# Kernel optimization log

Measured on AMD Instinct MI355X. Metric: run time of the kernel, lower is better.

The kernel has to match this reference:

```python
import jax, jax.numpy as jnp
import numpy as np

B, N, DI, DS, DP, DM, S = 64, 4096, 64, 64, 64, 128, 7
NUM_ITER = 3
EPS_ATTN = 1e-8
LN_EPS = 1e-5


def setup_inputs() -> dict:
    key = jax.random.key(0)
    ks = jax.random.split(key, 12)
    rn = lambda k, shp, sc=1.0: (jax.random.normal(k, shp, jnp.float32) * sc)
    return {
        "x": rn(ks[0], (B, N, DI)),
        "ln_inp_g": jnp.ones((DI,), jnp.float32),
        "ln_inp_b": jnp.zeros((DI,), jnp.float32),
        "ln_slot_g": jnp.ones((DS,), jnp.float32),
        "ln_slot_b": jnp.zeros((DS,), jnp.float32),
        "slots_init": rn(ks[1], (1, S, DS)),
        "Wk": rn(ks[2], (DI, DP), 1.0 / np.sqrt(DI)),
        "Wv": rn(ks[3], (DI, DP), 1.0 / np.sqrt(DI)),
        "Wq": rn(ks[4], (DS, DP), 1.0 / np.sqrt(DS)),
        "gru_wih": rn(ks[5], (3 * DS, DP), 1.0 / np.sqrt(DS)),
        "gru_whh": rn(ks[6], (3 * DS, DS), 1.0 / np.sqrt(DS)),
        "gru_bih": jnp.zeros((3 * DS,), jnp.float32),
        "gru_bhh": jnp.zeros((3 * DS,), jnp.float32),
        "mlp_w1": rn(ks[7], (DS, DM), 1.0 / np.sqrt(DS)),
        "mlp_b1": jnp.zeros((DM,), jnp.float32),
        "mlp_w2": rn(ks[8], (DM, DS), 1.0 / np.sqrt(DM)),
        "mlp_b2": jnp.zeros((DS,), jnp.float32),
    }


def _layernorm(x, g, b):
    m = jnp.mean(x, axis=-1, keepdims=True)
    v = jnp.mean(jnp.square(x - m), axis=-1, keepdims=True)
    return (x - m) * jax.lax.rsqrt(v + LN_EPS) * g + b


def _gru_cell(u, h, wih, whh, bih, bhh):
    # PyTorch GRUCell semantics
    gi = u @ wih.T + bih  # [*, 3*DS]
    gh = h @ whh.T + bhh
    ir, iz, inn = jnp.split(gi, 3, axis=-1)
    hr, hz, hn = jnp.split(gh, 3, axis=-1)
    r = jax.nn.sigmoid(ir + hr)
    z = jax.nn.sigmoid(iz + hz)
    n = jnp.tanh(inn + r * hn)
    return (1.0 - z) * n + z * h


def reference(x, ln_inp_g, ln_inp_b, ln_slot_g, ln_slot_b, slots_init,
              Wk, Wv, Wq, gru_wih, gru_whh, gru_bih, gru_bhh,
              mlp_w1, mlp_b1, mlp_w2, mlp_b2):
    x = _layernorm(x, ln_inp_g, ln_inp_b)          # [B,N,DI]
    k = x @ Wk                                      # [B,N,DP] (hoisted; x fixed across iters)
    v = x @ Wv                                      # [B,N,DP]
    slots = jnp.broadcast_to(slots_init, (x.shape[0], S, DS))
    scale = 1.0 / np.sqrt(DP)
    for _ in range(NUM_ITER):
        slots_prev = slots
        sn = _layernorm(slots, ln_slot_g, ln_slot_b)
        q = sn @ Wq                                 # [B,S,DP]
        attn = jnp.einsum('bnd,bsd->bns', k, q) * scale
        attn = jax.nn.softmax(attn, axis=-1) + EPS_ATTN      # softmax over slots
        weights = attn / jnp.sum(attn, axis=1, keepdims=True)  # normalize over N
        updates = jnp.einsum('bns,bnd->bsd', weights, v)     # [B,S,DP]
        h = _gru_cell(updates.reshape(-1, DP), slots_prev.reshape(-1, DS),
                      gru_wih, gru_whh, gru_bih, gru_bhh)
        slots = h.reshape(-1, S, DS)
        slots = slots + (jax.nn.relu(slots @ mlp_w1 + mlp_b1) @ mlp_w2 + mlp_b2)
    return slots
```

## Files before the change

### kernel.cpp

```cpp
#include <hip/hip_runtime.h>
#include <stdint.h>

#define L2E 1.44269504088896f

static __device__ __forceinline__ float wsum(float v) {
    #pragma unroll
    for (int m = 1; m < 64; m <<= 1) v += __shfl_xor(v, m, 64);
    return v;
}
static __device__ __forceinline__ float sigm(float x) {
    return 1.0f / (1.0f + __builtin_amdgcn_exp2f(-x * L2E));
}
static __device__ __forceinline__ float tanh_(float x) {
    const float ax = fabsf(x);
    const float t = __builtin_amdgcn_exp2f(-2.0f * ax * L2E);
    const float r = (1.0f - t) / (1.0f + t);
    return (x < 0.f) ? -r : r;
}

__global__ __launch_bounds__(256) void transpose_kernel(
    const float* __restrict__ wih, const float* __restrict__ whh,
    const float* __restrict__ Wk,
    float* __restrict__ wihT, float* __restrict__ whhT, float* __restrict__ WkT)
{
    const int idx = blockIdx.x * 256 + threadIdx.x;
    if (idx < 12288) {
        const int i = idx / 192, j = idx - i * 192;
        wihT[idx] = wih[j * 64 + i];
    } else if (idx < 24576) {
        const int o = idx - 12288;
        const int i = o / 192, j = o - i * 192;
        whhT[o] = whh[j * 64 + i];
    } else {
        const int o = idx - 24576;
        const int p = o >> 6, d = o & 63;
        WkT[o] = Wk[d * 64 + p];
    }
}

static __device__ __forceinline__ void slot_ln_q_kq(
    float snv, int wv, int lane, int r,
    float* scr, const float* wkT,
    const float* lsg, const float* lsb, const float* Wq,
    const float* lig, const float* lib,
    float* __restrict__ gkq, float* __restrict__ aux)
{
    const float mean = wsum(snv) * (1.0f / 64.0f);
    const float d = snv - mean;
    const float var = wsum(d * d) * (1.0f / 64.0f);
    const float rs = rsqrtf(var + 1e-5f);
    const float sn = d * rs * lsg[lane] + lsb[lane];
    __syncthreads();
    scr[lane] = sn;
    __syncthreads();
    float q = 0.f;
    #pragma unroll 8
    for (int i = 0; i < 64; ++i) q = fmaf(scr[i], Wq[i * 64 + lane], q);
    q *= 0.125f;
    __syncthreads();
    scr[lane] = q;
    __syncthreads();
    float kq = 0.f;
    #pragma unroll 8
    for (int p = 0; p < 64; ++p) kq = fmaf(wkT[p * 64 + lane], scr[p], kq);
    const float bk = wsum(lib[lane] * kq);
    const float gk = lig[lane] * kq;
    const float g1 = wsum(gk);
    gkq[r * 64 + lane] = gk;
    if (lane == 0) { aux[r * 2] = g1; aux[r * 2 + 1] = bk; }
}

__global__ __launch_bounds__(256) void init_kernel(
    const float* __restrict__ s0,
    const float* __restrict__ lsg, const float* __restrict__ lsb,
    const float* __restrict__ Wq,  const float* __restrict__ Wk,
    const float* __restrict__ lig, const float* __restrict__ lib,
    float* __restrict__ slots, float* __restrict__ gkq, float* __restrict__ aux)
{
    __shared__ float wkT[4096];
    __shared__ float scr[4][64];
    const int tid = threadIdx.x, lane = tid & 63, wv = tid >> 6;
    const int r = blockIdx.x * 4 + wv;
    const int s = r % 7;
    #pragma unroll
    for (int i = tid; i < 4096; i += 256) {
        const int d = i >> 6, p = i & 63;
        wkT[p * 64 + d] = Wk[i];
    }
    const float h = s0[s * 64 + lane];
    slots[r * 64 + lane] = h;
    __syncthreads();
    slot_ln_q_kq(h, wv, lane, r, &scr[wv][0], wkT, lsg, lsb, Wq, lig, lib, gkq, aux);
}

__global__ __launch_bounds__(256) void attn_kernel(
    const float* __restrict__ x,
    const float* __restrict__ gkq, const float* __restrict__ aux,
    float* __restrict__ Ypart)
{
    __shared__ float xsh[4][32 * 65];
    __shared__ float wsh[4][32][8];
    __shared__ float gkql[448];
    __shared__ float auxl[14];
    __shared__ float ybuf[4][456];
    const int tid = threadIdx.x, lane = tid & 63, wv = tid >> 6;
    const int b = blockIdx.x >> 4, chunk = blockIdx.x & 15;

    gkql[tid] = gkq[b * 448 + tid];
    if (tid < 192) gkql[tid + 256] = gkq[b * 448 + tid + 256];
    if (tid < 14) auxl[tid] = aux[b * 14 + tid];
    __syncthreads();

    const int q5 = lane & 31, h = lane >> 5;
    float Yr[14];
    #pragma unroll
    for (int i = 0; i < 14; ++i) Yr[i] = 0.f;
    float cacc[7] = {0.f, 0.f, 0.f, 0.f, 0.f, 0.f, 0.f};

    const float* tbase = x + (((long)b * 4096) + chunk * 256 + wv * 64) * 64;
    #pragma unroll 1
    for (int pass = 0; pass < 2; ++pass) {
        const float4* src = (const float4*)(tbase + pass * 2048);
        #pragma unroll
        for (int st = 0; st < 8; ++st) {
            const float4 d4 = src[st * 64 + lane];
            const int f = (st * 64 + lane) * 4;
            const int row = f >> 6, dim = f & 63;
            float* dst = &xsh[wv][row * 65 + dim];
            dst[0] = d4.x; dst[1] = d4.y; dst[2] = d4.z; dst[3] = d4.w;
        }

        float xf[32];
        float sum = 0.f, ss = 0.f;
        const float* xr = &xsh[wv][q5 * 65 + h * 32];
        #pragma unroll
        for (int c = 0; c < 32; ++c) {
            xf[c] = xr[c];
            sum += xf[c];
            ss = fmaf(xf[c], xf[c], ss);
        }
        float acc[7];
        #pragma unroll
        for (int s = 0; s < 7; ++s) {
            float a = 0.f;
            const float* gk = &gkql[s * 64 + h * 32];
            #pragma unroll
            for (int c = 0; c < 32; ++c) a = fmaf(xf[c], gk[c], a);
            acc[s] = a;
        }
        sum += __shfl_xor(sum, 32, 64);
        ss  += __shfl_xor(ss, 32, 64);
        #pragma unroll
        for (int s = 0; s < 7; ++s) acc[s] += __shfl_xor(acc[s], 32, 64);

        const float m   = sum * (1.0f / 64.0f);
        const float var = ss * (1.0f / 64.0f) - m * m;
        const float rs  = rsqrtf(var + 1e-5f);
        const float rsm = rs * m;
        float t[7];
        #pragma unroll
        for (int s = 0; s < 7; ++s)
            t[s] = fmaf(rs, acc[s], fmaf(-rsm, auxl[2 * s], auxl[2 * s + 1]));
        float mx = t[0];
        #pragma unroll
        for (int s = 1; s < 7; ++s) mx = fmaxf(mx, t[s]);
        float e[7], se = 0.f;
        #pragma unroll
        for (int s = 0; s < 7; ++s) {
            e[s] = __builtin_amdgcn_exp2f((t[s] - mx) * L2E);
            se += e[s];
        }
        const float inv = 1.0f / se;
        #pragma unroll
        for (int s = 0; s < 7; ++s) {
            const float w = fmaf(e[s], inv, 1e-8f);
            cacc[s] += w;
            if (h == 0) wsh[wv][q5][s] = w * rs;
        }
        if (h == 0) wsh[wv][q5][7] = 0.f;

        #pragma unroll 4
        for (int r2 = 0; r2 < 16; ++r2) {
            const int rr = r2 * 2 + h;
            const float4 p0 = *(const float4*)&wsh[wv][rr][0];
            const float4 p1 = *(const float4*)&wsh[wv][rr][4];
            const float v0 = xsh[wv][rr * 65 + q5 * 2];
            const float v1 = xsh[wv][rr * 65 + q5 * 2 + 1];
            const float ps[7] = {p0.x, p0.y, p0.z, p0.w, p1.x, p1.y, p1.z};
            #pragma unroll
            for (int s = 0; s < 7; ++s) {
                Yr[2 * s]     = fmaf(ps[s], v0, Yr[2 * s]);
                Yr[2 * s + 1] = fmaf(ps[s], v1, Yr[2 * s + 1]);
            }
        }
    }

    #pragma unroll
    for (int i = 0; i < 14; ++i) Yr[i] += __shfl_xor(Yr[i], 32, 64);
    if (h == 0) {
        #pragma unroll
        for (int s = 0; s < 7; ++s) {
            ybuf[wv][s * 64 + q5 * 2]     = Yr[2 * s];
            ybuf[wv][s * 64 + q5 * 2 + 1] = Yr[2 * s + 1];
        }
    }
    #pragma unroll
    for (int s = 0; s < 7; ++s) {
        const float Cs = wsum(cacc[s]) * 0.5f;
        if (lane == 0) ybuf[wv][448 + s] = Cs;
    }
    if (lane == 1) ybuf[wv][455] = 0.f;
    __syncthreads();
    for (int i = tid; i < 456; i += 256)
        Ypart[((long)b * 16 + chunk) * 456 + i] =
            ybuf[0][i] + ybuf[1][i] + ybuf[2][i] + ybuf[3][i];
}

__global__ __launch_bounds__(256) void update_kernel(
    const float* __restrict__ Ypart, float* __restrict__ slots,
    const float* __restrict__ Wv,
    const float* __restrict__ wihT, const float* __restrict__ whhT,
    const float* __restrict__ bih,  const float* __restrict__ bhh,
    const float* __restrict__ w1,   const float* __restrict__ b1,
    const float* __restrict__ w2,   const float* __restrict__ b2,
    const float* __restrict__ lsg,  const float* __restrict__ lsb,
    const float* __restrict__ Wq,   const float* __restrict__ WkT,
    const float* __restrict__ lig,  const float* __restrict__ lib,
    float* __restrict__ gkq, float* __restrict__ aux,
    float* __restrict__ out, int last)
{
    __shared__ float red[4][64];
    __shared__ float c16[16];
    __shared__ float ash[64];
    __shared__ float ush[64];
    __shared__ float hsh[64];
    __shared__ float gish[192], ghsh[192];
    __shared__ float hnsh[64];
    __shared__ float mbsh[128];
    __shared__ float qsh[64];
    const int tid = threadIdx.x, lane = tid & 63, wv = tid >> 6;
    const int r = blockIdx.x;
    const int b = r / 7, s = r - b * 7;
    const float* Yb = Ypart + (long)b * 16 * 456;

    float yp = 0.f;
    #pragma unroll
    for (int c = 0; c < 4; ++c)
        yp += Yb[(wv * 4 + c) * 456 + s * 64 + lane];
    red[wv][lane] = yp;
    if (tid < 16) c16[tid] = Yb[tid * 456 + 448 + s];
    if (tid >= 64 && tid < 128) hsh[tid - 64] = slots[r * 64 + (tid - 64)];
    __syncthreads();

    if (tid < 64) {
        const float Yd = red[0][lane] + red[1][lane] + red[2][lane] + red[3][lane];
        float C = 0.f;
        #pragma unroll
        for (int c = 0; c < 16; ++c) C += c16[c];
        const float Z = wsum(Yd) * (1.0f / 64.0f);
        ash[lane] = (lig[lane] * (Yd - Z) + lib[lane] * C) / C;
    }
    __syncthreads();

    float up = 0.f;
    #pragma unroll
    for (int i = 0; i < 16; ++i) {
        const int ii = wv * 16 + i;
        up = fmaf(ash[ii], Wv[ii * 64 + lane], up);
    }
    red[wv][lane] = up;
    __syncthreads();
    if (tid < 64) ush[lane] = red[0][lane] + red[1][lane] + red[2][lane] + red[3][lane];
    __syncthreads();

    if (tid < 192) {
        float a1 = bih[tid], a2 = bhh[tid];
        #pragma unroll 8
        for (int i = 0; i < 64; ++i) {
            a1 = fmaf(ush[i], wihT[i * 192 + tid], a1);
            a2 = fmaf(hsh[i], whhT[i * 192 + tid], a2);
        }
        gish[tid] = a1; ghsh[tid] = a2;
    }
    __syncthreads();
    if (tid < 64) {
        const float rr = sigm(gish[tid] + ghsh[tid]);
        const float zz = sigm(gish[64 + tid] + ghsh[64 + tid]);
        const float nn = tanh_(gish[128 + tid] + rr * ghsh[128 + tid]);
        hnsh[tid] = (1.f - zz) * nn + zz * hsh[tid];
    }
    __syncthreads();

    if (tid < 128) {
        float m = b1[tid];
        #pragma unroll 8
        for (int i = 0; i < 64; ++i) m = fmaf(hnsh[i], w1[i * 128 + tid], m);
        mbsh[tid] = fmaxf(m, 0.f);
    }
    __syncthreads();

    if (tid < 64) {
        float o = b2[tid];
        #pragma unroll 8
        for (int t = 0; t < 128; ++t) o = fmaf(mbsh[t], w2[t * 64 + tid], o);
        const float snv = hnsh[tid] + o;
        slots[r * 64 + tid] = snv;
        if (last) {
            out[r * 64 + tid] = snv;
        } else {
            const float mean = wsum(snv) * (1.0f / 64.0f);
            const float d = snv - mean;
            const float var = wsum(d * d) * (1.0f / 64.0f);
            const float rs = rsqrtf(var + 1e-5f);
            const float sn = d * rs * lsg[tid] + lsb[tid];
            ash[tid] = sn;
            float q = 0.f;
            #pragma unroll 8
            for (int i = 0; i < 64; ++i) q = fmaf(ash[i], Wq[i * 64 + tid], q);
            qsh[tid] = q * 0.125f;
            float kq = 0.f;
            #pragma unroll 8
            for (int p = 0; p < 64; ++p) kq = fmaf(WkT[p * 64 + tid], qsh[p], kq);
            const float bk = wsum(lib[tid] * kq);
            const float gk = lig[tid] * kq;
            const float g1 = wsum(gk);
            gkq[r * 64 + tid] = gk;
            if (tid == 0) { aux[r * 2] = g1; aux[r * 2 + 1] = bk; }
        }
    }
}

extern "C" void kernel_launch(void* const* d_in, const int* in_sizes, int n_in,
                              void* d_out, int out_size, void* d_ws, size_t ws_size,
                              hipStream_t stream)
{
    const float* x   = (const float*)d_in[0];
    const float* lig = (const float*)d_in[1];
    const float* lib = (const float*)d_in[2];
    const float* lsg = (const float*)d_in[3];
    const float* lsb = (const float*)d_in[4];
    const float* s0  = (const float*)d_in[5];
    const float* Wk  = (const float*)d_in[6];
    const float* Wv  = (const float*)d_in[7];
    const float* Wq  = (const float*)d_in[8];
    const float* wih = (const float*)d_in[9];
    const float* whh = (const float*)d_in[10];
    const float* bih = (const float*)d_in[11];
    const float* bhh = (const float*)d_in[12];
    const float* w1  = (const float*)d_in[13];
    const float* b1  = (const float*)d_in[14];
    const float* w2  = (const float*)d_in[15];
    const float* b2  = (const float*)d_in[16];

    float* f = (float*)d_ws;
    float* gkq   = f; f += 448 * 64;
    float* aux   = f; f += 448 * 2;
    float* slots = f; f += 448 * 64;
    float* Ypart = f; f += (long)64 * 16 * 456;
    float* wihT  = f; f += 64 * 192;
    float* whhT  = f; f += 64 * 192;
    float* WkT   = f; f += 64 * 64;

    transpose_kernel<<<112, 256, 0, stream>>>(wih, whh, Wk, wihT, whhT, WkT);
    init_kernel<<<112, 256, 0, stream>>>(s0, lsg, lsb, Wq, Wk, lig, lib,
                                         slots, gkq, aux);
    for (int it = 0; it < 3; ++it) {
        attn_kernel<<<1024, 256, 0, stream>>>(x, gkq, aux, Ypart);
        update_kernel<<<448, 256, 0, stream>>>(
            Ypart, slots, Wv, wihT, whhT, bih, bhh, w1, b1, w2, b2,
            lsg, lsb, Wq, WkT, lig, lib, gkq, aux,
            (float*)d_out, it == 2);
    }
}
```

Baseline: 236.8 us.

## Fuse slot update into attention kernel via last-block atomic counter and prefetch second pass

Merges the transpose kernel into the init kernel and folds the per-batch GRU/MLP/slot-LN update into the attention kernel. The last of the 16 chunk blocks per batch, found with an atomic counter, performs the update with one wave per slot. This removes four kernel launches and the Ypart round trip between kernels. The attention kernel also loads the second pass of x into registers before computing the first pass, and uses wave barriers with per-wave shared scratch instead of block syncs. The risks are a serialized tail on the winning block and extra register pressure from the prefetch, under a tighter launch bound.

```diff
diff --git a/kernel.cpp b/kernel.cpp
--- a/kernel.cpp
+++ b/kernel.cpp
@@ -18,12 +18,21 @@
     return (x < 0.f) ? -r : r;
 }
 
-__global__ __launch_bounds__(256) void transpose_kernel(
+__global__ __launch_bounds__(256) void init_kernel(
+    const float* __restrict__ s0,
+    const float* __restrict__ lsg, const float* __restrict__ lsb,
+    const float* __restrict__ Wq,  const float* __restrict__ Wk,
+    const float* __restrict__ lig, const float* __restrict__ lib,
     const float* __restrict__ wih, const float* __restrict__ whh,
-    const float* __restrict__ Wk,
-    float* __restrict__ wihT, float* __restrict__ whhT, float* __restrict__ WkT)
-{
-    const int idx = blockIdx.x * 256 + threadIdx.x;
+    float* __restrict__ slots, float* __restrict__ gkq, float* __restrict__ aux,
+    float* __restrict__ wihT, float* __restrict__ whhT, float* __restrict__ WkT,
+    int* __restrict__ cnt)
+{
+    __shared__ float wkT[4096];
+    __shared__ float scr[4][64];
+    const int tid = threadIdx.x, lane = tid & 63, wv = tid >> 6;
+    const int idx = blockIdx.x * 256 + tid;
+
     if (idx < 12288) {
         const int i = idx / 192, j = idx - i * 192;
         wihT[idx] = wih[j * 64 + i];
@@ -36,33 +45,36 @@
         const int p = o >> 6, d = o & 63;
         WkT[o] = Wk[d * 64 + p];
     }
-}
-
-static __device__ __forceinline__ void slot_ln_q_kq(
-    float snv, int wv, int lane, int r,
-    float* scr, const float* wkT,
-    const float* lsg, const float* lsb, const float* Wq,
-    const float* lig, const float* lib,
-    float* __restrict__ gkq, float* __restrict__ aux)
-{
-    const float mean = wsum(snv) * (1.0f / 64.0f);
-    const float d = snv - mean;
+    if (idx < 64) cnt[idx] = 0;
+
+    const int r = blockIdx.x * 4 + wv;
+    const int s = r % 7;
+    #pragma unroll
+    for (int i = tid; i < 4096; i += 256) {
+        const int d = i >> 6, p = i & 63;
+        wkT[p * 64 + d] = Wk[i];
+    }
+    const float h = s0[s * 64 + lane];
+    slots[r * 64 + lane] = h;
+    __syncthreads();
+
+    const float mean = wsum(h) * (1.0f / 64.0f);
+    const float d = h - mean;
     const float var = wsum(d * d) * (1.0f / 64.0f);
     const float rs = rsqrtf(var + 1e-5f);
     const float sn = d * rs * lsg[lane] + lsb[lane];
-    __syncthreads();
-    scr[lane] = sn;
+    scr[wv][lane] = sn;
     __syncthreads();
     float q = 0.f;
     #pragma unroll 8
-    for (int i = 0; i < 64; ++i) q = fmaf(scr[i], Wq[i * 64 + lane], q);
+    for (int i = 0; i < 64; ++i) q = fmaf(scr[wv][i], Wq[i * 64 + lane], q);
     q *= 0.125f;
     __syncthreads();
-    scr[lane] = q;
+    scr[wv][lane] = q;
     __syncthreads();
     float kq = 0.f;
     #pragma unroll 8
-    for (int p = 0; p < 64; ++p) kq = fmaf(wkT[p * 64 + lane], scr[p], kq);
+    for (int p = 0; p < 64; ++p) kq = fmaf(wkT[p * 64 + lane], scr[wv][p], kq);
     const float bk = wsum(lib[lane] * kq);
     const float gk = lig[lane] * kq;
     const float g1 = wsum(gk);
@@ -70,154 +82,93 @@
     if (lane == 0) { aux[r * 2] = g1; aux[r * 2 + 1] = bk; }
 }
 
-__global__ __launch_bounds__(256) void init_kernel(
-    const float* __restrict__ s0,
-    const float* __restrict__ lsg, const float* __restrict__ lsb,
-    const float* __restrict__ Wq,  const float* __restrict__ Wk,
-    const float* __restrict__ lig, const float* __restrict__ lib,
-    float* __restrict__ slots, float* __restrict__ gkq, float* __restrict__ aux)
-{
-    __shared__ float wkT[4096];
-    __shared__ float scr[4][64];
-    const int tid = threadIdx.x, lane = tid & 63, wv = tid >> 6;
-    const int r = blockIdx.x * 4 + wv;
-    const int s = r % 7;
-    #pragma unroll
-    for (int i = tid; i < 4096; i += 256) {
-        const int d = i >> 6, p = i & 63;
-        wkT[p * 64 + d] = Wk[i];
-    }
-    const float h = s0[s * 64 + lane];
-    slots[r * 64 + lane] = h;
-    __syncthreads();
-    slot_ln_q_kq(h, wv, lane, r, &scr[wv][0], wkT, lsg, lsb, Wq, lig, lib, gkq, aux);
-}
-
-__global__ __launch_bounds__(256) void attn_kernel(
+static __device__ __forceinline__ void stage_store(float* xw, const float4* R, int lane)
+{
+    #pragma unroll
+    for (int st = 0; st < 8; ++st) {
+        const int row = st * 4 + (lane >> 4);
+        const int dim = (lane & 15) * 4;
+        float* d = xw + row * 65 + dim;
+        d[0] = R[st].x; d[1] = R[st].y; d[2] = R[st].z; d[3] = R[st].w;
+    }
+}
+
+static __device__ __forceinline__ void do_pass(
+    float* __restrict__ xw, float* __restrict__ wshw,
+    const float* __restrict__ gkql, const float* __restrict__ auxl,
+    int q5, int h, float* Yr, float* cacc)
+{
+    float xf[32];
+    float sum = 0.f, ss = 0.f;
+    const float* xr = xw + q5 * 65 + h * 32;
+    #pragma unroll
+    for (int c = 0; c < 32; ++c) {
+        xf[c] = xr[c];
+        sum += xf[c];
+        ss = fmaf(xf[c], xf[c], ss);
+    }
+    float acc[7];
+    #pragma unroll
+    for (int s = 0; s < 7; ++s) {
+        float a = 0.f;
+        const float* gk = &gkql[s * 64 + h * 32];
+        #pragma unroll
+        for (int c = 0; c < 32; ++c) a = fmaf(xf[c], gk[c], a);
+        acc[s] = a;
+    }
+    sum += __shfl_xor(sum, 32, 64);
+    ss  += __shfl_xor(ss, 32, 64);
+    #pragma unroll
+    for (int s = 0; s < 7; ++s) acc[s] += __shfl_xor(acc[s], 32, 64);
+
+    const float m   = sum * (1.0f / 64.0f);
+    const float var = ss * (1.0f / 64.0f) - m * m;
+    const float rs  = rsqrtf(var + 1e-5f);
+    const float rsm = rs * m;
+    float t[7];
+    #pragma unroll
+    for (int s = 0; s < 7; ++s)
+        t[s] = fmaf(rs, acc[s], fmaf(-rsm, auxl[2 * s], auxl[2 * s + 1]));
+    float mx = t[0];
+    #pragma unroll
+    for (int s = 1; s < 7; ++s) mx = fmaxf(mx, t[s]);
+    float e[7], se = 0.f;
+    #pragma unroll
+    for (int s = 0; s < 7; ++s) {
+        e[s] = __builtin_amdgcn_exp2f((t[s] - mx) * L2E);
+        se += e[s];
+    }
+    const float inv = 1.0f / se;
+    #pragma unroll
+    for (int s = 0; s < 7; ++s) {
+        const float w = fmaf(e[s], inv, 1e-8f);
+        cacc[s] += w;
+        if (h == 0) wshw[q5 * 8 + s] = w * rs;
+    }
+    if (h == 0) wshw[q5 * 8 + 7] = 0.f;
+    __builtin_amdgcn_wave_barrier();
+
+    #pragma unroll 4
+    for (int r2 = 0; r2 < 16; ++r2) {
+        const int rr = r2 * 2 + h;
+        const float4 p0 = *(const float4*)&wshw[rr * 8];
+        const float4 p1 = *(const float4*)&wshw[rr * 8 + 4];
+        const float v0 = xw[rr * 65 + q5 * 2];
+        const float v1 = xw[rr * 65 + q5 * 2 + 1];
+        const float ps[7] = {p0.x, p0.y, p0.z, p0.w, p1.x, p1.y, p1.z};
+        #pragma unroll
+        for (int s = 0; s < 7; ++s) {
+            Yr[2 * s]     = fmaf(ps[s], v0, Yr[2 * s]);
+            Yr[2 * s + 1] = fmaf(ps[s], v1, Yr[2 * s + 1]);
+        }
+    }
+}
+
+__global__ __launch_bounds__(256, 4) void attn_kernel(
     const float* __restrict__ x,
-    const float* __restrict__ gkq, const float* __restrict__ aux,
-    float* __restrict__ Ypart)
-{
-    __shared__ float xsh[4][32 * 65];
-    __shared__ float wsh[4][32][8];
-    __shared__ float gkql[448];
-    __shared__ float auxl[14];
-    __shared__ float ybuf[4][456];
-    const int tid = threadIdx.x, lane = tid & 63, wv = tid >> 6;
-    const int b = blockIdx.x >> 4, chunk = blockIdx.x & 15;
-
-    gkql[tid] = gkq[b * 448 + tid];
-    if (tid < 192) gkql[tid + 256] = gkq[b * 448 + tid + 256];
-    if (tid < 14) auxl[tid] = aux[b * 14 + tid];
-    __syncthreads();
-
-    const int q5 = lane & 31, h = lane >> 5;
-    float Yr[14];
-    #pragma unroll
-    for (int i = 0; i < 14; ++i) Yr[i] = 0.f;
-    float cacc[7] = {0.f, 0.f, 0.f, 0.f, 0.f, 0.f, 0.f};
-
-    const float* tbase = x + (((long)b * 4096) + chunk * 256 + wv * 64) * 64;
-    #pragma unroll 1
-    for (int pass = 0; pass < 2; ++pass) {
-        const float4* src = (const float4*)(tbase + pass * 2048);
-        #pragma unroll
-        for (int st = 0; st < 8; ++st) {
-            const float4 d4 = src[st * 64 + lane];
-            const int f = (st * 64 + lane) * 4;
-            const int row = f >> 6, dim = f & 63;
-            float* dst = &xsh[wv][row * 65 + dim];
-            dst[0] = d4.x; dst[1] = d4.y; dst[2] = d4.z; dst[3] = d4.w;
-        }
-
-        float xf[32];
-        float sum = 0.f, ss = 0.f;
-        const float* xr = &xsh[wv][q5 * 65 + h * 32];
-        #pragma unroll
-        for (int c = 0; c < 32; ++c) {
-            xf[c] = xr[c];
-            sum += xf[c];
-            ss = fmaf(xf[c], xf[c], ss);
-        }
-        float acc[7];
-        #pragma unroll
-        for (int s = 0; s < 7; ++s) {
-            float a = 0.f;
-            const float* gk = &gkql[s * 64 + h * 32];
-            #pragma unroll
-            for (int c = 0; c < 32; ++c) a = fmaf(xf[c], gk[c], a);
-            acc[s] = a;
-        }
-        sum += __shfl_xor(sum, 32, 64);
-        ss  += __shfl_xor(ss, 32, 64);
-        #pragma unroll
-        for (int s = 0; s < 7; ++s) acc[s] += __shfl_xor(acc[s], 32, 64);
-
-        const float m   = sum * (1.0f / 64.0f);
-        const float var = ss * (1.0f / 64.0f) - m * m;
-        const float rs  = rsqrtf(var + 1e-5f);
-        const float rsm = rs * m;
-        float t[7];
-        #pragma unroll
-        for (int s = 0; s < 7; ++s)
-            t[s] = fmaf(rs, acc[s], fmaf(-rsm, auxl[2 * s], auxl[2 * s + 1]));
-        float mx = t[0];
-        #pragma unroll
-        for (int s = 1; s < 7; ++s) mx = fmaxf(mx, t[s]);
-        float e[7], se = 0.f;
-        #pragma unroll
-        for (int s = 0; s < 7; ++s) {
-            e[s] = __builtin_amdgcn_exp2f((t[s] - mx) * L2E);
-            se += e[s];
-        }
-        const float inv = 1.0f / se;
-        #pragma unroll
-        for (int s = 0; s < 7; ++s) {
-            const float w = fmaf(e[s], inv, 1e-8f);
-            cacc[s] += w;
-            if (h == 0) wsh[wv][q5][s] = w * rs;
-        }
-        if (h == 0) wsh[wv][q5][7] = 0.f;
-
-        #pragma unroll 4
-        for (int r2 = 0; r2 < 16; ++r2) {
-            const int rr = r2 * 2 + h;
-            const float4 p0 = *(const float4*)&wsh[wv][rr][0];
-            const float4 p1 = *(const float4*)&wsh[wv][rr][4];
-            const float v0 = xsh[wv][rr * 65 + q5 * 2];
-            const float v1 = xsh[wv][rr * 65 + q5 * 2 + 1];
-            const float ps[7] = {p0.x, p0.y, p0.z, p0.w, p1.x, p1.y, p1.z};
-            #pragma unroll
-            for (int s = 0; s < 7; ++s) {
-                Yr[2 * s]     = fmaf(ps[s], v0, Yr[2 * s]);
-                Yr[2 * s + 1] = fmaf(ps[s], v1, Yr[2 * s + 1]);
-            }
-        }
-    }
-
-    #pragma unroll
-    for (int i = 0; i < 14; ++i) Yr[i] += __shfl_xor(Yr[i], 32, 64);
-    if (h == 0) {
-        #pragma unroll
-        for (int s = 0; s < 7; ++s) {
-            ybuf[wv][s * 64 + q5 * 2]     = Yr[2 * s];
-            ybuf[wv][s * 64 + q5 * 2 + 1] = Yr[2 * s + 1];
-        }
-    }
-    #pragma unroll
-    for (int s = 0; s < 7; ++s) {
-        const float Cs = wsum(cacc[s]) * 0.5f;
-        if (lane == 0) ybuf[wv][448 + s] = Cs;
-    }
-    if (lane == 1) ybuf[wv][455] = 0.f;
-    __syncthreads();
-    for (int i = tid; i < 456; i += 256)
-        Ypart[((long)b * 16 + chunk) * 456 + i] =
-            ybuf[0][i] + ybuf[1][i] + ybuf[2][i] + ybuf[3][i];
-}
-
-__global__ __launch_bounds__(256) void update_kernel(
-    const float* __restrict__ Ypart, float* __restrict__ slots,
+    float* __restrict__ gkq, float* __restrict__ aux,
+    float* __restrict__ Ypart, int* __restrict__ cnt,
+    float* __restrict__ slots,
     const float* __restrict__ Wv,
     const float* __restrict__ wihT, const float* __restrict__ whhT,
     const float* __restrict__ bih,  const float* __restrict__ bhh,
@@ -226,106 +177,161 @@
     const float* __restrict__ lsg,  const float* __restrict__ lsb,
     const float* __restrict__ Wq,   const float* __restrict__ WkT,
     const float* __restrict__ lig,  const float* __restrict__ lib,
-    float* __restrict__ gkq, float* __restrict__ aux,
     float* __restrict__ out, int last)
 {
-    __shared__ float red[4][64];
-    __shared__ float c16[16];
-    __shared__ float ash[64];
-    __shared__ float ush[64];
-    __shared__ float hsh[64];
-    __shared__ float gish[192], ghsh[192];
-    __shared__ float hnsh[64];
-    __shared__ float mbsh[128];
-    __shared__ float qsh[64];
+    __shared__ float xsh[4][2080];
+    __shared__ float wsh[4][256];
+    __shared__ float gkql[448];
+    __shared__ float auxl[14];
+    __shared__ int winflag;
     const int tid = threadIdx.x, lane = tid & 63, wv = tid >> 6;
-    const int r = blockIdx.x;
-    const int b = r / 7, s = r - b * 7;
+    const int b = blockIdx.x >> 4, chunk = blockIdx.x & 15;
+
+    gkql[tid] = gkq[b * 448 + tid];
+    if (tid < 192) gkql[tid + 256] = gkq[b * 448 + tid + 256];
+    if (tid < 14) auxl[tid] = aux[b * 14 + tid];
+    __syncthreads();
+
+    const int q5 = lane & 31, h = lane >> 5;
+    float Yr[14];
+    #pragma unroll
+    for (int i = 0; i < 14; ++i) Yr[i] = 0.f;
+    float cacc[7] = {0.f, 0.f, 0.f, 0.f, 0.f, 0.f, 0.f};
+
+    float* xw = &xsh[wv][0];
+    float* wshw = &wsh[wv][0];
+    const float* tbase = x + (((long)b * 4096) + chunk * 256 + wv * 64) * 64;
+
+    {
+        const float4* srcA = (const float4*)tbase;
+        float4 Ra[8];
+        #pragma unroll
+        for (int st = 0; st < 8; ++st) Ra[st] = srcA[st * 64 + lane];
+        stage_store(xw, Ra, lane);
+    }
+    float4 Rb[8];
+    {
+        const float4* srcB = (const float4*)(tbase + 2048);
+        #pragma unroll
+        for (int st = 0; st < 8; ++st) Rb[st] = srcB[st * 64 + lane];
+    }
+    do_pass(xw, wshw, gkql, auxl, q5, h, Yr, cacc);
+    __builtin_amdgcn_wave_barrier();
+    stage_store(xw, Rb, lane);
+    do_pass(xw, wshw, gkql, auxl, q5, h, Yr, cacc);
+
+    #pragma unroll
+    for (int i = 0; i < 14; ++i) Yr[i] += __shfl_xor(Yr[i], 32, 64);
+    __builtin_amdgcn_wave_barrier();
+    if (h == 0) {
+        #pragma unroll
+        for (int s = 0; s < 7; ++s) {
+            xw[s * 64 + q5 * 2]     = Yr[2 * s];
+            xw[s * 64 + q5 * 2 + 1] = Yr[2 * s + 1];
+        }
+    }
+    #pragma unroll
+    for (int s = 0; s < 7; ++s) {
+        const float Cs = wsum(cacc[s]) * 0.5f;
+        if (lane == 0) xw[448 + s] = Cs;
+    }
+    __syncthreads();
+    for (int i = tid; i < 455; i += 256)
+        Ypart[((long)b * 16 + chunk) * 456 + i] =
+            xsh[0][i] + xsh[1][i] + xsh[2][i] + xsh[3][i];
+
+    __threadfence();
+    if (tid == 0) winflag = (atomicAdd(&cnt[b], 1) == 15) ? 1 : 0;
+    __syncthreads();
+    if (!winflag) return;
+    __threadfence();
+    if (tid == 0) cnt[b] = 0;
+
     const float* Yb = Ypart + (long)b * 16 * 456;
-
-    float yp = 0.f;
-    #pragma unroll
-    for (int c = 0; c < 4; ++c)
-        yp += Yb[(wv * 4 + c) * 456 + s * 64 + lane];
-    red[wv][lane] = yp;
-    if (tid < 16) c16[tid] = Yb[tid * 456 + 448 + s];
-    if (tid >= 64 && tid < 128) hsh[tid - 64] = slots[r * 64 + (tid - 64)];
-    __syncthreads();
-
-    if (tid < 64) {
-        const float Yd = red[0][lane] + red[1][lane] + red[2][lane] + red[3][lane];
-        float C = 0.f;
-        #pragma unroll
-        for (int c = 0; c < 16; ++c) C += c16[c];
+    float* sw = &xsh[wv][0];
+    #pragma unroll 1
+    for (int si = 0; si < 2; ++si) {
+        const int s = wv + si * 4;
+        if (s >= 7) break;
+        const int r = b * 7 + s;
+
+        float Yd = 0.f, C = 0.f;
+        #pragma unroll
+        for (int c = 0; c < 16; ++c) {
+            Yd += Yb[c * 456 + s * 64 + lane];
+            C  += Yb[c * 456 + 448 + s];
+        }
         const float Z = wsum(Yd) * (1.0f / 64.0f);
-        ash[lane] = (lig[lane] * (Yd - Z) + lib[lane] * C) / C;
-    }
-    __syncthreads();
-
-    float up = 0.f;
-    #pragma unroll
-    for (int i = 0; i < 16; ++i) {
-        const int ii = wv * 16 + i;
-        up = fmaf(ash[ii], Wv[ii * 64 + lane], up);
-    }
-    red[wv][lane] = up;
-    __syncthreads();
-    if (tid < 64) ush[lane] = red[0][lane] + red[1][lane] + red[2][lane] + red[3][lane];
-    __syncthreads();
-
-    if (tid < 192) {
-        float a1 = bih[tid], a2 = bhh[tid];
+        const float aoc = (lig[lane] * (Yd - Z) + lib[lane] * C) / C;
+        sw[lane] = aoc;
+        __builtin_amdgcn_wave_barrier();
+        float u = 0.f;
+        #pragma unroll 8
+        for (int i = 0; i < 64; ++i) u = fmaf(sw[i], Wv[i * 64 + lane], u);
+        const float hv = slots[r * 64 + lane];
+        __builtin_amdgcn_wave_barrier();
+        sw[64 + lane] = u; sw[128 + lane] = hv;
+        __builtin_amdgcn_wave_barrier();
+
+        float gi[3], gh[3];
+        #pragma unroll
+        for (int g = 0; g < 3; ++g) {
+            const int j = g * 64 + lane;
+            float a1 = bih[j], a2 = bhh[j];
+            #pragma unroll 8
+            for (int i = 0; i < 64; ++i) {
+                a1 = fmaf(sw[64 + i],  wihT[i * 192 + j], a1);
+                a2 = fmaf(sw[128 + i], whhT[i * 192 + j], a2);
+            }
+            gi[g] = a1; gh[g] = a2;
+        }
+        const float rr = sigm(gi[0] + gh[0]);
+        const float zz = sigm(gi[1] + gh[1]);
+        const float nn = tanh_(gi[2] + rr * gh[2]);
+        const float hn = (1.f - zz) * nn + zz * hv;
+        sw[192 + lane] = hn;
+        __builtin_amdgcn_wave_barrier();
+
+        float m0 = b1[lane], m1 = b1[64 + lane];
         #pragma unroll 8
         for (int i = 0; i < 64; ++i) {
-            a1 = fmaf(ush[i], wihT[i * 192 + tid], a1);
-            a2 = fmaf(hsh[i], whhT[i * 192 + tid], a2);
-        }
-        gish[tid] = a1; ghsh[tid] = a2;
-    }
-    __syncthreads();
-    if (tid < 64) {
-        const float rr = sigm(gish[tid] + ghsh[tid]);
-        const float zz = sigm(gish[64 + tid] + ghsh[64 + tid]);
-        const float nn = tanh_(gish[128 + tid] + rr * ghsh[128 + tid]);
-        hnsh[tid] = (1.f - zz) * nn + zz * hsh[tid];
-    }
-    __syncthreads();
-
-    if (tid < 128) {
-        float m = b1[tid];
+            const float hni = sw[192 + i];
+            m0 = fmaf(hni, w1[i * 128 + lane], m0);
+            m1 = fmaf(hni, w1[i * 128 + 64 + lane], m1);
+        }
+        m0 = fmaxf(m0, 0.f); m1 = fmaxf(m1, 0.f);
+        sw[256 + lane] = m0; sw[320 + lane] = m1;
+        __builtin_amdgcn_wave_barrier();
+        float o = b2[lane];
         #pragma unroll 8
-        for (int i = 0; i < 64; ++i) m = fmaf(hnsh[i], w1[i * 128 + tid], m);
-        mbsh[tid] = fmaxf(m, 0.f);
-    }
-    __syncthreads();
-
-    if (tid < 64) {
-        float o = b2[tid];
-        #pragma unroll 8
-        for (int t = 0; t < 128; ++t) o = fmaf(mbsh[t], w2[t * 64 + tid], o);
-        const float snv = hnsh[tid] + o;
-        slots[r * 64 + tid] = snv;
+        for (int t = 0; t < 128; ++t) o = fmaf(sw[256 + t], w2[t * 64 + lane], o);
+        const float snv = hn + o;
+        slots[r * 64 + lane] = snv;
+
         if (last) {
-            out[r * 64 + tid] = snv;
+            out[r * 64 + lane] = snv;
         } else {
             const float mean = wsum(snv) * (1.0f / 64.0f);
             const float d = snv - mean;
             const float var = wsum(d * d) * (1.0f / 64.0f);
             const float rs = rsqrtf(var + 1e-5f);
-            const float sn = d * rs * lsg[tid] + lsb[tid];
-            ash[tid] = sn;
+            const float sn = d * rs * lsg[lane] + lsb[lane];
+            sw[384 + lane] = sn;
+            __builtin_amdgcn_wave_barrier();
             float q = 0.f;
             #pragma unroll 8
-            for (int i = 0; i < 64; ++i) q = fmaf(ash[i], Wq[i * 64 + tid], q);
-            qsh[tid] = q * 0.125f;
+            for (int i = 0; i < 64; ++i) q = fmaf(sw[384 + i], Wq[i * 64 + lane], q);
+            sw[448 + lane] = q * 0.125f;
+            __builtin_amdgcn_wave_barrier();
             float kq = 0.f;
             #pragma unroll 8
-            for (int p = 0; p < 64; ++p) kq = fmaf(WkT[p * 64 + tid], qsh[p], kq);
-            const float bk = wsum(lib[tid] * kq);
-            const float gk = lig[tid] * kq;
+            for (int p = 0; p < 64; ++p) kq = fmaf(WkT[p * 64 + lane], sw[448 + p], kq);
+            const float bk = wsum(lib[lane] * kq);
+            const float gk = lig[lane] * kq;
             const float g1 = wsum(gk);
-            gkq[r * 64 + tid] = gk;
-            if (tid == 0) { aux[r * 2] = g1; aux[r * 2 + 1] = bk; }
+            gkq[r * 64 + lane] = gk;
+            if (lane == 0) { aux[r * 2] = g1; aux[r * 2 + 1] = bk; }
+            __builtin_amdgcn_wave_barrier();
         }
     }
 }
@@ -360,15 +366,15 @@
     float* wihT  = f; f += 64 * 192;
     float* whhT  = f; f += 64 * 192;
     float* WkT   = f; f += 64 * 64;
-
-    transpose_kernel<<<112, 256, 0, stream>>>(wih, whh, Wk, wihT, whhT, WkT);
+    int*   cnt   = (int*)f; f += 64;
+
     init_kernel<<<112, 256, 0, stream>>>(s0, lsg, lsb, Wq, Wk, lig, lib,
-                                         slots, gkq, aux);
+                                         wih, whh, slots, gkq, aux,
+                                         wihT, whhT, WkT, cnt);
     for (int it = 0; it < 3; ++it) {
-        attn_kernel<<<1024, 256, 0, stream>>>(x, gkq, aux, Ypart);
-        update_kernel<<<448, 256, 0, stream>>>(
-            Ypart, slots, Wv, wihT, whhT, bih, bhh, w1, b1, w2, b2,
-            lsg, lsb, Wq, WkT, lig, lib, gkq, aux,
+        attn_kernel<<<1024, 256, 0, stream>>>(
+            x, gkq, aux, Ypart, cnt, slots, Wv, wihT, whhT, bih, bhh,
+            w1, b1, w2, b2, lsg, lsb, Wq, WkT, lig, lib,
             (float*)d_out, it == 2);
     }
 }
```

New measurement: 523.4 us. +121.0%, slower.
